# Performance work log

Measured on AMD Instinct MI355X. Metric: run time of the kernel, lower is better.

The kernel has to match this reference:

```python
import jax, jax.numpy as jnp
import numpy as np

# Episode configuration (matches init_kwargs); feature map fixed by module: [64,7,7]
N_WAY, K_SHOT, Q_QUERY, PRJ = 10, 5, 100, 16
DIM, H, W = 64, 7, 7
N_SUP = N_WAY * K_SHOT * PRJ      # 800 support samples
N_QRY = N_WAY * Q_QUERY * PRJ     # 16000 query samples
B = N_SUP + N_QRY                 # 16800
TRIU_I, TRIU_J = np.triu_indices(DIM)  # row-major upper-tri indices, matches torch nonzero order


def setup_inputs() -> dict:
    key = jax.random.key(0)
    k1, k2 = jax.random.split(key)
    feat = jax.random.normal(k1, (B, DIM, H, W), dtype=jnp.float32)
    label = jax.random.randint(k2, (N_QRY,), 0, N_WAY, dtype=jnp.int64)
    # nn.Parameter init: log(1/(2*h*w)) * ones(1,1)
    temp = jnp.log(jnp.ones((1, 1), dtype=jnp.float32) / (2.0 * H * W))
    return {"feat": feat, "temp": temp, "label": label}


def _bdcovpool(x, t):
    # x: [B, dim, h, w] -> Brownian distance covariance matrix [B, dim, dim]
    b, d, h, w = x.shape
    xm = x.reshape(b, d, h * w)
    g = jnp.einsum('bim,bjm->bij', xm, xm)            # x @ x^T, [B,d,d]
    dg = jnp.diagonal(g, axis1=1, axis2=2)            # [B,d]
    # I_M @ (G*I) + (G*I) @ I_M - 2G  ==  diag_j + diag_i - 2G
    dcov = dg[:, None, :] + dg[:, :, None] - 2.0 * g
    dcov = jnp.sqrt(jnp.exp(t) * jnp.clip(dcov, 0.0) + 1e-5)
    # double centering: dcov - rowmean - colmean + totalmean
    rm = jnp.mean(dcov, axis=2, keepdims=True)        # (1/d) dcov @ I_M
    cm = jnp.mean(dcov, axis=1, keepdims=True)        # (1/d) I_M @ dcov
    tm = jnp.mean(dcov, axis=(1, 2), keepdims=True)   # (1/d^2) I_M @ dcov @ I_M
    return dcov - rm - cm + tm


def reference(feat, temp, label):
    v = _bdcovpool(feat, temp)                        # [B, 64, 64]
    tv = v[:, TRIU_I, TRIU_J]                         # Triuvec: [B, 2080]
    support = tv[:N_SUP].reshape(N_WAY, K_SHOT * PRJ, -1).mean(axis=1)  # [n_way, 2080]
    query = tv[N_SUP:]                                # [N_QRY, 2080]
    # negative squared euclidean distance (expanded form of sum((x-y)^2))
    q2 = jnp.sum(query * query, axis=1, keepdims=True)          # [N_QRY,1]
    s2 = jnp.sum(support * support, axis=1)[None, :]             # [1,n_way]
    score = -(q2 + s2 - 2.0 * jnp.einsum('nd,md->nm', query, support))  # [N_QRY, n_way]
    logp = jax.nn.log_softmax(score, axis=-1)
    loss = -jnp.mean(jnp.take_along_axis(logp, label[:, None], axis=1))
    return score, loss
```

## Files before the change

### kernel.cpp

```cpp
#include <hip/hip_runtime.h>
#include <math.h>

#define NWAY   10
#define DIMD   64
#define HWN    49
#define NSUP   800
#define NQRY   16000
#define NTRI   2080
#define FEAT_PER (DIMD*HWN)
#define STP    12

typedef __attribute__((ext_vector_type(8))) short bf16x8;
typedef __attribute__((ext_vector_type(4))) float f32x4;

struct __align__(16) BDCShared {
    union {
        unsigned short hl[2*DIMD*64];
        float dcov[DIMD*64];
        float part[256*12];
    } u;
    float dg[DIMD];
    float rm[DIMD];
    float w4[4];
    float red[16];
};

__device__ __forceinline__ void k2ij(int k, int& io, int& jo) {
    int ii = (int)floorf((129.0f - sqrtf(16641.0f - 8.0f*(float)k)) * 0.5f);
    int off = ii*(129-ii)/2;
    if (off > k) { --ii; off = ii*(129-ii)/2; }
    else {
        int off2 = (ii+1)*(128-ii)/2;
        if (off2 <= k) { ii += 1; off = off2; }
    }
    io = ii;
    jo = ii + (k - off);
}

__device__ __forceinline__ unsigned cvt_pk_bf16(float a, float b) {
    unsigned r;
    asm("v_cvt_pk_bf16_f32 %0, %1, %2" : "=v"(r) : "v"(a), "v"(b));
    return r;
}

#define HL_ADDR(BASE, row, e) \
    ((BASE) + (row)*64 + (((((e) >> 3) ^ ((row) & 7))) << 3))

__device__ __forceinline__ float bdc_compute(const float* __restrict__ feat,
                                             float et, int sample, BDCShared& sm,
                                             f32x4& v0, f32x4& v1, f32x4& v2,
                                             f32x4& v3) {
    const int tid = threadIdx.x;
    unsigned short* Hh = sm.u.hl;
    unsigned short* Lh = sm.u.hl + DIMD*64;

    {
        const int d = tid & 63, hq = tid >> 6;
        const float* rowp = feat + (size_t)sample * FEAT_PER + d*HWN + hq*16;
        float x[16];
        if (hq < 3) {
            #pragma unroll
            for (int i = 0; i < 16; ++i) x[i] = rowp[i];
        } else {
            x[0] = rowp[0];
            #pragma unroll
            for (int i = 1; i < 16; ++i) x[i] = 0.0f;
        }
        unsigned hp[8], lp[8];
        #pragma unroll
        for (int i = 0; i < 8; ++i) {
            unsigned h = cvt_pk_bf16(x[2*i], x[2*i+1]);
            float h0 = __uint_as_float(h << 16);
            float h1 = __uint_as_float(h & 0xffff0000u);
            hp[i] = h;
            lp[i] = cvt_pk_bf16(x[2*i] - h0, x[2*i+1] - h1);
        }
        const int sw0 = (hq*2)     ^ (d & 7);
        const int sw1 = (hq*2 + 1) ^ (d & 7);
        *(uint4*)&Hh[d*64 + sw0*8] = make_uint4(hp[0], hp[1], hp[2], hp[3]);
        *(uint4*)&Hh[d*64 + sw1*8] = make_uint4(hp[4], hp[5], hp[6], hp[7]);
        *(uint4*)&Lh[d*64 + sw0*8] = make_uint4(lp[0], lp[1], lp[2], lp[3]);
        *(uint4*)&Lh[d*64 + sw1*8] = make_uint4(lp[4], lp[5], lp[6], lp[7]);
    }
    __syncthreads();

    const int wv = tid >> 6, lane = tid & 63;
    const int qd = lane >> 4, c15 = lane & 15;
    const int rA = 16*wv + c15;
    bf16x8 AH0 = *(const bf16x8*)HL_ADDR(Hh, rA, qd*8);
    bf16x8 AH1 = *(const bf16x8*)HL_ADDR(Hh, rA, qd*8 + 32);
    bf16x8 AL0 = *(const bf16x8*)HL_ADDR(Lh, rA, qd*8);
    bf16x8 AL1 = *(const bf16x8*)HL_ADDR(Lh, rA, qd*8 + 32);

    f32x4 acc[4];
    #pragma unroll
    for (int J = 0; J < 4; ++J) {
        const int rB = 16*J + c15;
        bf16x8 BH0 = *(const bf16x8*)HL_ADDR(Hh, rB, qd*8);
        bf16x8 BH1 = *(const bf16x8*)HL_ADDR(Hh, rB, qd*8 + 32);
        bf16x8 BL0 = *(const bf16x8*)HL_ADDR(Lh, rB, qd*8);
        bf16x8 BL1 = *(const bf16x8*)HL_ADDR(Lh, rB, qd*8 + 32);
        f32x4 a = {0.f, 0.f, 0.f, 0.f};
        a = __builtin_amdgcn_mfma_f32_16x16x32_bf16(AH0, BH0, a, 0, 0, 0);
        a = __builtin_amdgcn_mfma_f32_16x16x32_bf16(AH1, BH1, a, 0, 0, 0);
        a = __builtin_amdgcn_mfma_f32_16x16x32_bf16(AL0, BH0, a, 0, 0, 0);
        a = __builtin_amdgcn_mfma_f32_16x16x32_bf16(AL1, BH1, a, 0, 0, 0);
        a = __builtin_amdgcn_mfma_f32_16x16x32_bf16(AH0, BL0, a, 0, 0, 0);
        a = __builtin_amdgcn_mfma_f32_16x16x32_bf16(AH1, BL1, a, 0, 0, 0);
        acc[J] = a;
    }

    #pragma unroll
    for (int J = 0; J < 4; ++J) {
        if (J == wv) {
            #pragma unroll
            for (int r = 0; r < 4; ++r)
                if (c15 == 4*qd + r) sm.dg[16*wv + c15] = acc[J][r];
        }
    }
    __syncthreads();

    f32x4 dgi = *(const f32x4*)&sm.dg[16*wv + 4*qd];
    float rs0 = 0.f, rs1 = 0.f, rs2 = 0.f, rs3 = 0.f;
#define DCOV_J(J, VJ)                                                          \
    {   float dgj = sm.dg[16*(J) + c15];                                       \
        _Pragma("unroll")                                                      \
        for (int r = 0; r < 4; ++r) {                                          \
            float t2 = fmaf(-2.0f, acc[J][r], dgi[r] + dgj);                   \
            t2 = fmaxf(t2, 0.0f);                                              \
            VJ[r] = __builtin_amdgcn_sqrtf(fmaf(et, t2, 1e-5f));               \
        }                                                                      \
        rs0 += VJ[0]; rs1 += VJ[1]; rs2 += VJ[2]; rs3 += VJ[3]; }
    DCOV_J(0, v0)
    DCOV_J(1, v1)
    DCOV_J(2, v2)
    DCOV_J(3, v3)
#undef DCOV_J

    #pragma unroll
    for (int off = 1; off < 16; off <<= 1) {
        rs0 += __shfl_xor(rs0, off, 64);
        rs1 += __shfl_xor(rs1, off, 64);
        rs2 += __shfl_xor(rs2, off, 64);
        rs3 += __shfl_xor(rs3, off, 64);
    }
    if (c15 == 0) {
        f32x4 rmv = {rs0*(1.0f/64.0f), rs1*(1.0f/64.0f),
                     rs2*(1.0f/64.0f), rs3*(1.0f/64.0f)};
        *(f32x4*)&sm.rm[16*wv + 4*qd] = rmv;
    }
    float tt = (rs0 + rs1) + (rs2 + rs3);
    tt += __shfl_xor(tt, 16, 64);
    tt += __shfl_xor(tt, 32, 64);
    if (lane == 0) sm.w4[wv] = tt;
    __syncthreads();
    float tm = (sm.w4[0] + sm.w4[1] + sm.w4[2] + sm.w4[3]) * (1.0f/4096.0f);

    const float rmi0 = rs0*(1.0f/64.0f), rmi1 = rs1*(1.0f/64.0f),
                rmi2 = rs2*(1.0f/64.0f), rmi3 = rs3*(1.0f/64.0f);
    float* dcovf = sm.u.dcov;
    const int cch = 4*wv + qd;
#define CENTER_J(J, VJ)                                                        \
    {   int j16 = 16*(J) + c15;                                                \
        float rmj = sm.rm[j16] - tm;                                           \
        VJ[0] = VJ[0] - rmi0 - rmj;                                            \
        VJ[1] = VJ[1] - rmi1 - rmj;                                            \
        VJ[2] = VJ[2] - rmi2 - rmj;                                            \
        VJ[3] = VJ[3] - rmi3 - rmj;                                            \
        *(f32x4*)&dcovf[j16*64 + ((cch ^ (j16 & 7)) << 2)] = VJ; }
    CENTER_J(0, v0)
    CENTER_J(1, v1)
    CENTER_J(2, v2)
    CENTER_J(3, v3)
#undef CENTER_J
    __syncthreads();
    return tm;
}

__global__ void kern_init(unsigned* __restrict__ table,
                          float* __restrict__ s2,
                          float* __restrict__ loss_slot) {
    int i = blockIdx.x * 256 + threadIdx.x;
    if (i < NTRI) {
        int ii, jj; k2ij(i, ii, jj);
        unsigned faddr = (unsigned)(jj*64 + ((((ii >> 2) ^ (jj & 7)) << 2) | (ii & 3)));
        table[i] = (faddr << 16) | ((unsigned)ii << 8) | (unsigned)jj;
    }
    if (i < NWAY) s2[i] = 0.0f;
    if (i == 0) loss_slot[0] = 0.0f;
}

__global__ __launch_bounds__(256, 8) void kern_support(const float* __restrict__ feat,
                                                       const float* __restrict__ temp,
                                                       float* __restrict__ tvout) {
    __shared__ BDCShared sm;
    float et = __expf(temp[0]);
    int s = blockIdx.x;
    f32x4 v0, v1, v2, v3;
    bdc_compute(feat, et, s, sm, v0, v1, v2, v3);

    const int tid = threadIdx.x;
    const int wv = tid >> 6, lane = tid & 63;
    const int qd = lane >> 4, c15 = lane & 15;
    const int iB = 16*wv + 4*qd;
    float* dst = tvout + (size_t)s * NTRI;
#define SUP_J(J, VJ)                                                           \
    {   int j = 16*(J) + c15;                                                  \
        _Pragma("unroll")                                                      \
        for (int r = 0; r < 4; ++r) {                                          \
            int i = iB + r;                                                    \
            if (j >= i) dst[i*(129 - i)/2 + (j - i)] = VJ[r]; } }
    SUP_J(0, v0)
    SUP_J(1, v1)
    SUP_J(2, v2)
    SUP_J(3, v3)
#undef SUP_J
}

__global__ __launch_bounds__(256) void kern_reduce(const float* __restrict__ tv,
                                                   const unsigned* __restrict__ table,
                                                   float* __restrict__ supT,
                                                   float* __restrict__ s2) {
    __shared__ float red[4];
    int m = blockIdx.x / 9, kc = blockIdx.x % 9;
    int k = kc*256 + threadIdx.x;
    float S = 0.0f;
    if (k < NTRI) {
        const float* p = tv + (size_t)(80*m) * NTRI + k;
        float a0 = 0.f, a1 = 0.f, a2 = 0.f, a3 = 0.f;
        for (int s4 = 0; s4 < 80; s4 += 4) {
            a0 += p[(size_t)(s4+0)*NTRI];
            a1 += p[(size_t)(s4+1)*NTRI];
            a2 += p[(size_t)(s4+2)*NTRI];
            a3 += p[(size_t)(s4+3)*NTRI];
        }
        S = ((a0+a1)+(a2+a3)) * (1.0f/80.0f);
        supT[k*STP + m] = S;
    }
    float ps = S * S;
    int lane = threadIdx.x & 63, wv = threadIdx.x >> 6;
    #pragma unroll
    for (int off = 32; off > 0; off >>= 1) ps += __shfl_xor(ps, off, 64);
    if (lane == 0) red[wv] = ps;
    __syncthreads();
    if (threadIdx.x == 0) atomicAdd(&s2[m], red[0]+red[1]+red[2]+red[3]);
}

__global__ __launch_bounds__(256, 8) void kern_query(const float* __restrict__ feat,
                                                     const float* __restrict__ temp,
                                                     const unsigned* __restrict__ table,
                                                     const float* __restrict__ supT,
                                                     const float* __restrict__ s2,
                                                     float* __restrict__ out) {
    __shared__ BDCShared sm;
    float et = __expf(temp[0]);
    int qn = blockIdx.x;
    f32x4 v0, v1, v2, v3;
    bdc_compute(feat, et, NSUP + qn, sm, v0, v1, v2, v3);

    const int tid = threadIdx.x;
    float qq = 0.0f;
    float cr[NWAY];
    #pragma unroll
    for (int m = 0; m < NWAY; ++m) cr[m] = 0.0f;

    const float* dcov = sm.u.dcov;
    for (int k = tid; k < NTRI; k += 256) {
        unsigned t = table[k];
        float v = dcov[t >> 16];
        qq = fmaf(v, v, qq);
        const float4* sp = (const float4*)(supT + (size_t)k * STP);
        float4 sa = sp[0], sb = sp[1], sc = sp[2];
        cr[0] = fmaf(v, sa.x, cr[0]);
        cr[1] = fmaf(v, sa.y, cr[1]);
        cr[2] = fmaf(v, sa.z, cr[2]);
        cr[3] = fmaf(v, sa.w, cr[3]);
        cr[4] = fmaf(v, sb.x, cr[4]);
        cr[5] = fmaf(v, sb.y, cr[5]);
        cr[6] = fmaf(v, sb.z, cr[6]);
        cr[7] = fmaf(v, sb.w, cr[7]);
        cr[8] = fmaf(v, sc.x, cr[8]);
        cr[9] = fmaf(v, sc.y, cr[9]);
    }
    __syncthreads();

    float* part = sm.u.part;
    f32x4 p0 = {cr[0], cr[1], cr[2], cr[3]};
    f32x4 p1 = {cr[4], cr[5], cr[6], cr[7]};
    f32x4 p2 = {cr[8], cr[9], qq, 0.0f};
    *(f32x4*)&part[tid*12 + 0] = p0;
    *(f32x4*)&part[tid*12 + 4] = p1;
    *(f32x4*)&part[tid*12 + 8] = p2;
    __syncthreads();
    if (tid < 176) {
        int m = tid >> 4, g = tid & 15;
        float s = 0.0f;
        #pragma unroll
        for (int t = 0; t < 16; ++t) s += part[(g + 16*t)*12 + m];
        #pragma unroll
        for (int off = 1; off < 16; off <<= 1) s += __shfl_xor(s, off, 64);
        if (g == 0) sm.red[m] = s;
    }
    __syncthreads();
    if (tid < NWAY)
        out[(size_t)qn * NWAY + tid] = -(sm.red[10] + s2[tid] - 2.0f*sm.red[tid]);
}

__global__ __launch_bounds__(256) void kern_loss(const float* __restrict__ score,
                                                 const int* __restrict__ label,
                                                 float* __restrict__ loss_out) {
    __shared__ float red[4];
    int n = blockIdx.x * 256 + threadIdx.x;
    float lsum = 0.0f;
    if (n < NQRY) {
        const float* srow = score + (size_t)n * NWAY;
        float s[NWAY];
        float mx = -1e30f;
        #pragma unroll
        for (int m = 0; m < NWAY; ++m) { s[m] = srow[m]; mx = fmaxf(mx, s[m]); }
        float se = 0.0f;
        #pragma unroll
        for (int m = 0; m < NWAY; ++m) se += __expf(s[m] - mx);
        float lse = mx + __logf(se);
        lsum = lse - s[label[n]];
    }
    int lane = threadIdx.x & 63, wv = threadIdx.x >> 6;
    #pragma unroll
    for (int off = 32; off > 0; off >>= 1) lsum += __shfl_xor(lsum, off, 64);
    if (lane == 0) red[wv] = lsum;
    __syncthreads();
    if (threadIdx.x == 0)
        atomicAdd(loss_out, (red[0] + red[1] + red[2] + red[3]) * (1.0f / (float)NQRY));
}

extern "C" void kernel_launch(void* const* d_in, const int* in_sizes, int n_in,
                              void* d_out, int out_size, void* d_ws, size_t ws_size,
                              hipStream_t stream) {
    (void)in_sizes; (void)n_in; (void)out_size; (void)ws_size;
    const float* feat = (const float*)d_in[0];
    const float* temp = (const float*)d_in[1];
    const int*   label = (const int*)d_in[2];
    float* out = (float*)d_out;

    float*    tv    = (float*)d_ws;
    float*    supT  = tv + (size_t)NSUP * NTRI;
    float*    s2    = supT + NTRI*STP;
    unsigned* table = (unsigned*)(s2 + 16);
    float* loss_slot = out + (size_t)NQRY * NWAY;

    kern_init<<<(NTRI + 255)/256, 256, 0, stream>>>(table, s2, loss_slot);
    kern_support<<<NSUP, 256, 0, stream>>>(feat, temp, tv);
    kern_reduce<<<NWAY*9, 256, 0, stream>>>(tv, table, supT, s2);
    kern_query<<<NQRY, 256, 0, stream>>>(feat, temp, table, supT, s2, out);
    kern_loss<<<(NQRY + 255)/256, 256, 0, stream>>>(out, label, loss_slot);
}
```

Baseline: 351.2 us.

## Process two query samples per block in kern_query to amortize support loads

kern_query now handles two query samples per 256-thread block, staging both feature maps into double shared-memory regions and interleaving their Gram, dcov, centering and score accumulation. Each supT row and table entry loaded from global memory is reused for both queries, halving the support/table traffic and the number of barriers per sample. In exchange shared memory and register use roughly double, and launch bounds drop from 8 to 4 blocks per CU, which lowers occupancy and latency hiding.

Measured after the change: 337.4 us. 3.9% less time.

```diff
diff --git a/kernel.cpp b/kernel.cpp
--- a/kernel.cpp
+++ b/kernel.cpp
@@ -25,6 +25,20 @@
     float red[16];
 };
 
+struct __align__(16) BDC2Shared {
+    union Reg {
+        unsigned short hl[2*DIMD*64];
+        float dcov[DIMD*64];
+        float part[256*12];
+    };
+    Reg r0;
+    Reg r1;
+    float dg0[DIMD], dg1[DIMD];
+    float rm0[DIMD], rm1[DIMD];
+    float w40[4], w41[4];
+    float red0[16], red1[16];
+};
+
 __device__ __forceinline__ void k2ij(int k, int& io, int& jo) {
     int ii = (int)floorf((129.0f - sqrtf(16641.0f - 8.0f*(float)k)) * 0.5f);
     int off = ii*(129-ii)/2;
@@ -46,69 +60,93 @@
 #define HL_ADDR(BASE, row, e) \
     ((BASE) + (row)*64 + (((((e) >> 3) ^ ((row) & 7))) << 3))
 
+
+#define STAGE_Q(HLBASE, SAMPLE)                                                \
+    {   const float* rowp = feat + (size_t)(SAMPLE)*FEAT_PER + d*HWN + hq*16;  \
+        float x[16];                                                           \
+        if (hq < 3) {                                                          \
+            _Pragma("unroll")                                                  \
+            for (int i = 0; i < 16; ++i) x[i] = rowp[i];                       \
+        } else {                                                               \
+            x[0] = rowp[0];                                                    \
+            _Pragma("unroll")                                                  \
+            for (int i = 1; i < 16; ++i) x[i] = 0.0f;                          \
+        }                                                                      \
+        unsigned hp[8], lp[8];                                                 \
+        _Pragma("unroll")                                                      \
+        for (int i = 0; i < 8; ++i) {                                          \
+            unsigned h = cvt_pk_bf16(x[2*i], x[2*i+1]);                        \
+            float h0 = __uint_as_float(h << 16);                               \
+            float h1 = __uint_as_float(h & 0xffff0000u);                       \
+            hp[i] = h;                                                         \
+            lp[i] = cvt_pk_bf16(x[2*i] - h0, x[2*i+1] - h1);                   \
+        }                                                                      \
+        unsigned short* Hq = (HLBASE);                                         \
+        unsigned short* Lq = (HLBASE) + DIMD*64;                               \
+        *(uint4*)&Hq[d*64 + sw0*8] = make_uint4(hp[0], hp[1], hp[2], hp[3]);   \
+        *(uint4*)&Hq[d*64 + sw1*8] = make_uint4(hp[4], hp[5], hp[6], hp[7]);   \
+        *(uint4*)&Lq[d*64 + sw0*8] = make_uint4(lp[0], lp[1], lp[2], lp[3]);   \
+        *(uint4*)&Lq[d*64 + sw1*8] = make_uint4(lp[4], lp[5], lp[6], lp[7]); }
+
+#define GRAM_Q(HLBASE, ACC)                                                    \
+    {   unsigned short* Hq = (HLBASE);                                         \
+        unsigned short* Lq = (HLBASE) + DIMD*64;                               \
+        bf16x8 AH0 = *(const bf16x8*)HL_ADDR(Hq, rA, qd*8);                    \
+        bf16x8 AH1 = *(const bf16x8*)HL_ADDR(Hq, rA, qd*8 + 32);               \
+        bf16x8 AL0 = *(const bf16x8*)HL_ADDR(Lq, rA, qd*8);                    \
+        bf16x8 AL1 = *(const bf16x8*)HL_ADDR(Lq, rA, qd*8 + 32);               \
+        _Pragma("unroll")                                                      \
+        for (int J = 0; J < 4; ++J) {                                          \
+            const int rB = 16*J + c15;                                         \
+            bf16x8 BH0 = *(const bf16x8*)HL_ADDR(Hq, rB, qd*8);                \
+            bf16x8 BH1 = *(const bf16x8*)HL_ADDR(Hq, rB, qd*8 + 32);           \
+            bf16x8 BL0 = *(const bf16x8*)HL_ADDR(Lq, rB, qd*8);                \
+            bf16x8 BL1 = *(const bf16x8*)HL_ADDR(Lq, rB, qd*8 + 32);           \
+            f32x4 a = {0.f, 0.f, 0.f, 0.f};                                    \
+            a = __builtin_amdgcn_mfma_f32_16x16x32_bf16(AH0, BH0, a, 0, 0, 0); \
+            a = __builtin_amdgcn_mfma_f32_16x16x32_bf16(AH1, BH1, a, 0, 0, 0); \
+            a = __builtin_amdgcn_mfma_f32_16x16x32_bf16(AL0, BH0, a, 0, 0, 0); \
+            a = __builtin_amdgcn_mfma_f32_16x16x32_bf16(AL1, BH1, a, 0, 0, 0); \
+            a = __builtin_amdgcn_mfma_f32_16x16x32_bf16(AH0, BL0, a, 0, 0, 0); \
+            a = __builtin_amdgcn_mfma_f32_16x16x32_bf16(AH1, BL1, a, 0, 0, 0); \
+            ACC[J] = a;                                                        \
+        } }
+
+#define DCOV_J(J, VJ, ACC, DGARR, DGI, RS0, RS1, RS2, RS3)                     \
+    {   float dgj = (DGARR)[16*(J) + c15];                                     \
+        _Pragma("unroll")                                                      \
+        for (int r = 0; r < 4; ++r) {                                          \
+            float t2 = fmaf(-2.0f, ACC[J][r], (DGI)[r] + dgj);                 \
+            t2 = fmaxf(t2, 0.0f);                                              \
+            VJ[r] = __builtin_amdgcn_sqrtf(fmaf(et, t2, 1e-5f));               \
+        }                                                                      \
+        RS0 += VJ[0]; RS1 += VJ[1]; RS2 += VJ[2]; RS3 += VJ[3]; }
+
+#define CENTER_J(J, VJ, RMARR, DCOVF, TM, RMI0, RMI1, RMI2, RMI3)              \
+    {   int j16 = 16*(J) + c15;                                                \
+        float rmj = (RMARR)[j16] - (TM);                                       \
+        VJ[0] = VJ[0] - (RMI0) - rmj;                                          \
+        VJ[1] = VJ[1] - (RMI1) - rmj;                                          \
+        VJ[2] = VJ[2] - (RMI2) - rmj;                                          \
+        VJ[3] = VJ[3] - (RMI3) - rmj;                                          \
+        *(f32x4*)&(DCOVF)[j16*64 + ((cch ^ (j16 & 7)) << 2)] = VJ; }
+
 __device__ __forceinline__ float bdc_compute(const float* __restrict__ feat,
                                              float et, int sample, BDCShared& sm,
                                              f32x4& v0, f32x4& v1, f32x4& v2,
                                              f32x4& v3) {
     const int tid = threadIdx.x;
-    unsigned short* Hh = sm.u.hl;
-    unsigned short* Lh = sm.u.hl + DIMD*64;
-
-    {
-        const int d = tid & 63, hq = tid >> 6;
-        const float* rowp = feat + (size_t)sample * FEAT_PER + d*HWN + hq*16;
-        float x[16];
-        if (hq < 3) {
-            #pragma unroll
-            for (int i = 0; i < 16; ++i) x[i] = rowp[i];
-        } else {
-            x[0] = rowp[0];
-            #pragma unroll
-            for (int i = 1; i < 16; ++i) x[i] = 0.0f;
-        }
-        unsigned hp[8], lp[8];
-        #pragma unroll
-        for (int i = 0; i < 8; ++i) {
-            unsigned h = cvt_pk_bf16(x[2*i], x[2*i+1]);
-            float h0 = __uint_as_float(h << 16);
-            float h1 = __uint_as_float(h & 0xffff0000u);
-            hp[i] = h;
-            lp[i] = cvt_pk_bf16(x[2*i] - h0, x[2*i+1] - h1);
-        }
-        const int sw0 = (hq*2)     ^ (d & 7);
-        const int sw1 = (hq*2 + 1) ^ (d & 7);
-        *(uint4*)&Hh[d*64 + sw0*8] = make_uint4(hp[0], hp[1], hp[2], hp[3]);
-        *(uint4*)&Hh[d*64 + sw1*8] = make_uint4(hp[4], hp[5], hp[6], hp[7]);
-        *(uint4*)&Lh[d*64 + sw0*8] = make_uint4(lp[0], lp[1], lp[2], lp[3]);
-        *(uint4*)&Lh[d*64 + sw1*8] = make_uint4(lp[4], lp[5], lp[6], lp[7]);
-    }
+    const int d = tid & 63, hq = tid >> 6;
+    const int sw0 = (hq*2) ^ (d & 7);
+    const int sw1 = (hq*2 + 1) ^ (d & 7);
+    STAGE_Q(sm.u.hl, sample)
     __syncthreads();
 
     const int wv = tid >> 6, lane = tid & 63;
     const int qd = lane >> 4, c15 = lane & 15;
     const int rA = 16*wv + c15;
-    bf16x8 AH0 = *(const bf16x8*)HL_ADDR(Hh, rA, qd*8);
-    bf16x8 AH1 = *(const bf16x8*)HL_ADDR(Hh, rA, qd*8 + 32);
-    bf16x8 AL0 = *(const bf16x8*)HL_ADDR(Lh, rA, qd*8);
-    bf16x8 AL1 = *(const bf16x8*)HL_ADDR(Lh, rA, qd*8 + 32);
-
     f32x4 acc[4];
-    #pragma unroll
-    for (int J = 0; J < 4; ++J) {
-        const int rB = 16*J + c15;
-        bf16x8 BH0 = *(const bf16x8*)HL_ADDR(Hh, rB, qd*8);
-        bf16x8 BH1 = *(const bf16x8*)HL_ADDR(Hh, rB, qd*8 + 32);
-        bf16x8 BL0 = *(const bf16x8*)HL_ADDR(Lh, rB, qd*8);
-        bf16x8 BL1 = *(const bf16x8*)HL_ADDR(Lh, rB, qd*8 + 32);
-        f32x4 a = {0.f, 0.f, 0.f, 0.f};
-        a = __builtin_amdgcn_mfma_f32_16x16x32_bf16(AH0, BH0, a, 0, 0, 0);
-        a = __builtin_amdgcn_mfma_f32_16x16x32_bf16(AH1, BH1, a, 0, 0, 0);
-        a = __builtin_amdgcn_mfma_f32_16x16x32_bf16(AL0, BH0, a, 0, 0, 0);
-        a = __builtin_amdgcn_mfma_f32_16x16x32_bf16(AL1, BH1, a, 0, 0, 0);
-        a = __builtin_amdgcn_mfma_f32_16x16x32_bf16(AH0, BL0, a, 0, 0, 0);
-        a = __builtin_amdgcn_mfma_f32_16x16x32_bf16(AH1, BL1, a, 0, 0, 0);
-        acc[J] = a;
-    }
+    GRAM_Q(sm.u.hl, acc)
 
     #pragma unroll
     for (int J = 0; J < 4; ++J) {
@@ -122,20 +160,10 @@
 
     f32x4 dgi = *(const f32x4*)&sm.dg[16*wv + 4*qd];
     float rs0 = 0.f, rs1 = 0.f, rs2 = 0.f, rs3 = 0.f;
-#define DCOV_J(J, VJ)                                                          \
-    {   float dgj = sm.dg[16*(J) + c15];                                       \
-        _Pragma("unroll")                                                      \
-        for (int r = 0; r < 4; ++r) {                                          \
-            float t2 = fmaf(-2.0f, acc[J][r], dgi[r] + dgj);                   \
-            t2 = fmaxf(t2, 0.0f);                                              \
-            VJ[r] = __builtin_amdgcn_sqrtf(fmaf(et, t2, 1e-5f));               \
-        }                                                                      \
-        rs0 += VJ[0]; rs1 += VJ[1]; rs2 += VJ[2]; rs3 += VJ[3]; }
-    DCOV_J(0, v0)
-    DCOV_J(1, v1)
-    DCOV_J(2, v2)
-    DCOV_J(3, v3)
-#undef DCOV_J
+    DCOV_J(0, v0, acc, sm.dg, dgi, rs0, rs1, rs2, rs3)
+    DCOV_J(1, v1, acc, sm.dg, dgi, rs0, rs1, rs2, rs3)
+    DCOV_J(2, v2, acc, sm.dg, dgi, rs0, rs1, rs2, rs3)
+    DCOV_J(3, v3, acc, sm.dg, dgi, rs0, rs1, rs2, rs3)
 
     #pragma unroll
     for (int off = 1; off < 16; off <<= 1) {
@@ -160,19 +188,10 @@
                 rmi2 = rs2*(1.0f/64.0f), rmi3 = rs3*(1.0f/64.0f);
     float* dcovf = sm.u.dcov;
     const int cch = 4*wv + qd;
-#define CENTER_J(J, VJ)                                                        \
-    {   int j16 = 16*(J) + c15;                                                \
-        float rmj = sm.rm[j16] - tm;                                           \
-        VJ[0] = VJ[0] - rmi0 - rmj;                                            \
-        VJ[1] = VJ[1] - rmi1 - rmj;                                            \
-        VJ[2] = VJ[2] - rmi2 - rmj;                                            \
-        VJ[3] = VJ[3] - rmi3 - rmj;                                            \
-        *(f32x4*)&dcovf[j16*64 + ((cch ^ (j16 & 7)) << 2)] = VJ; }
-    CENTER_J(0, v0)
-    CENTER_J(1, v1)
-    CENTER_J(2, v2)
-    CENTER_J(3, v3)
-#undef CENTER_J
+    CENTER_J(0, v0, sm.rm, dcovf, tm, rmi0, rmi1, rmi2, rmi3)
+    CENTER_J(1, v1, sm.rm, dcovf, tm, rmi0, rmi1, rmi2, rmi3)
+    CENTER_J(2, v2, sm.rm, dcovf, tm, rmi0, rmi1, rmi2, rmi3)
+    CENTER_J(3, v3, sm.rm, dcovf, tm, rmi0, rmi1, rmi2, rmi3)
     __syncthreads();
     return tm;
 }
@@ -246,64 +265,175 @@
     if (threadIdx.x == 0) atomicAdd(&s2[m], red[0]+red[1]+red[2]+red[3]);
 }
 
-__global__ __launch_bounds__(256, 8) void kern_query(const float* __restrict__ feat,
+__global__ __launch_bounds__(256, 4) void kern_query(const float* __restrict__ feat,
                                                      const float* __restrict__ temp,
                                                      const unsigned* __restrict__ table,
                                                      const float* __restrict__ supT,
                                                      const float* __restrict__ s2,
                                                      float* __restrict__ out) {
-    __shared__ BDCShared sm;
+    __shared__ BDC2Shared sm;
     float et = __expf(temp[0]);
-    int qn = blockIdx.x;
-    f32x4 v0, v1, v2, v3;
-    bdc_compute(feat, et, NSUP + qn, sm, v0, v1, v2, v3);
-
+    const int qn0 = blockIdx.x * 2;
+    const int qn1 = qn0 + 1;
     const int tid = threadIdx.x;
-    float qq = 0.0f;
-    float cr[NWAY];
-    #pragma unroll
-    for (int m = 0; m < NWAY; ++m) cr[m] = 0.0f;
-
-    const float* dcov = sm.u.dcov;
+
+    {
+        const int d = tid & 63, hq = tid >> 6;
+        const int sw0 = (hq*2) ^ (d & 7);
+        const int sw1 = (hq*2 + 1) ^ (d & 7);
+        STAGE_Q(sm.r0.hl, NSUP + qn0)
+        STAGE_Q(sm.r1.hl, NSUP + qn1)
+    }
+    __syncthreads();
+
+    const int wv = tid >> 6, lane = tid & 63;
+    const int qd = lane >> 4, c15 = lane & 15;
+    const int rA = 16*wv + c15;
+    f32x4 acc0[4], acc1[4];
+    GRAM_Q(sm.r0.hl, acc0)
+    GRAM_Q(sm.r1.hl, acc1)
+
+    #pragma unroll
+    for (int J = 0; J < 4; ++J) {
+        if (J == wv) {
+            #pragma unroll
+            for (int r = 0; r < 4; ++r)
+                if (c15 == 4*qd + r) {
+                    sm.dg0[16*wv + c15] = acc0[J][r];
+                    sm.dg1[16*wv + c15] = acc1[J][r];
+                }
+        }
+    }
+    __syncthreads();
+
+    f32x4 dgi0 = *(const f32x4*)&sm.dg0[16*wv + 4*qd];
+    f32x4 dgi1 = *(const f32x4*)&sm.dg1[16*wv + 4*qd];
+    f32x4 v00, v01, v02, v03, v10, v11, v12, v13;
+    float rs00 = 0.f, rs01 = 0.f, rs02 = 0.f, rs03 = 0.f;
+    float rs10 = 0.f, rs11 = 0.f, rs12 = 0.f, rs13 = 0.f;
+    DCOV_J(0, v00, acc0, sm.dg0, dgi0, rs00, rs01, rs02, rs03)
+    DCOV_J(1, v01, acc0, sm.dg0, dgi0, rs00, rs01, rs02, rs03)
+    DCOV_J(2, v02, acc0, sm.dg0, dgi0, rs00, rs01, rs02, rs03)
+    DCOV_J(3, v03, acc0, sm.dg0, dgi0, rs00, rs01, rs02, rs03)
+    DCOV_J(0, v10, acc1, sm.dg1, dgi1, rs10, rs11, rs12, rs13)
+    DCOV_J(1, v11, acc1, sm.dg1, dgi1, rs10, rs11, rs12, rs13)
+    DCOV_J(2, v12, acc1, sm.dg1, dgi1, rs10, rs11, rs12, rs13)
+    DCOV_J(3, v13, acc1, sm.dg1, dgi1, rs10, rs11, rs12, rs13)
+
+    #pragma unroll
+    for (int off = 1; off < 16; off <<= 1) {
+        rs00 += __shfl_xor(rs00, off, 64);
+        rs01 += __shfl_xor(rs01, off, 64);
+        rs02 += __shfl_xor(rs02, off, 64);
+        rs03 += __shfl_xor(rs03, off, 64);
+        rs10 += __shfl_xor(rs10, off, 64);
+        rs11 += __shfl_xor(rs11, off, 64);
+        rs12 += __shfl_xor(rs12, off, 64);
+        rs13 += __shfl_xor(rs13, off, 64);
+    }
+    if (c15 == 0) {
+        f32x4 rmv0 = {rs00*(1.0f/64.0f), rs01*(1.0f/64.0f),
+                      rs02*(1.0f/64.0f), rs03*(1.0f/64.0f)};
+        f32x4 rmv1 = {rs10*(1.0f/64.0f), rs11*(1.0f/64.0f),
+                      rs12*(1.0f/64.0f), rs13*(1.0f/64.0f)};
+        *(f32x4*)&sm.rm0[16*wv + 4*qd] = rmv0;
+        *(f32x4*)&sm.rm1[16*wv + 4*qd] = rmv1;
+    }
+    float tt0 = (rs00 + rs01) + (rs02 + rs03);
+    float tt1 = (rs10 + rs11) + (rs12 + rs13);
+    tt0 += __shfl_xor(tt0, 16, 64);
+    tt0 += __shfl_xor(tt0, 32, 64);
+    tt1 += __shfl_xor(tt1, 16, 64);
+    tt1 += __shfl_xor(tt1, 32, 64);
+    if (lane == 0) { sm.w40[wv] = tt0; sm.w41[wv] = tt1; }
+    __syncthreads();
+    float tm0 = (sm.w40[0] + sm.w40[1] + sm.w40[2] + sm.w40[3]) * (1.0f/4096.0f);
+    float tm1 = (sm.w41[0] + sm.w41[1] + sm.w41[2] + sm.w41[3]) * (1.0f/4096.0f);
+
+    {
+        const float rmi00 = rs00*(1.0f/64.0f), rmi01 = rs01*(1.0f/64.0f),
+                    rmi02 = rs02*(1.0f/64.0f), rmi03 = rs03*(1.0f/64.0f);
+        const float rmi10 = rs10*(1.0f/64.0f), rmi11 = rs11*(1.0f/64.0f),
+                    rmi12 = rs12*(1.0f/64.0f), rmi13 = rs13*(1.0f/64.0f);
+        float* dc0 = sm.r0.dcov;
+        float* dc1 = sm.r1.dcov;
+        const int cch = 4*wv + qd;
+        CENTER_J(0, v00, sm.rm0, dc0, tm0, rmi00, rmi01, rmi02, rmi03)
+        CENTER_J(1, v01, sm.rm0, dc0, tm0, rmi00, rmi01, rmi02, rmi03)
+        CENTER_J(2, v02, sm.rm0, dc0, tm0, rmi00, rmi01, rmi02, rmi03)
+        CENTER_J(3, v03, sm.rm0, dc0, tm0, rmi00, rmi01, rmi02, rmi03)
+        CENTER_J(0, v10, sm.rm1, dc1, tm1, rmi10, rmi11, rmi12, rmi13)
+        CENTER_J(1, v11, sm.rm1, dc1, tm1, rmi10, rmi11, rmi12, rmi13)
+        CENTER_J(2, v12, sm.rm1, dc1, tm1, rmi10, rmi11, rmi12, rmi13)
+        CENTER_J(3, v13, sm.rm1, dc1, tm1, rmi10, rmi11, rmi12, rmi13)
+    }
+    __syncthreads();
+
+    float qq0 = 0.0f, qq1 = 0.0f;
+    float cr0[NWAY], cr1[NWAY];
+    #pragma unroll
+    for (int m = 0; m < NWAY; ++m) { cr0[m] = 0.0f; cr1[m] = 0.0f; }
+
+    const float* dcov0 = sm.r0.dcov;
+    const float* dcov1 = sm.r1.dcov;
     for (int k = tid; k < NTRI; k += 256) {
         unsigned t = table[k];
-        float v = dcov[t >> 16];
-        qq = fmaf(v, v, qq);
+        float va = dcov0[t >> 16];
+        float vb = dcov1[t >> 16];
+        qq0 = fmaf(va, va, qq0);
+        qq1 = fmaf(vb, vb, qq1);
         const float4* sp = (const float4*)(supT + (size_t)k * STP);
         float4 sa = sp[0], sb = sp[1], sc = sp[2];
-        cr[0] = fmaf(v, sa.x, cr[0]);
-        cr[1] = fmaf(v, sa.y, cr[1]);
-        cr[2] = fmaf(v, sa.z, cr[2]);
-        cr[3] = fmaf(v, sa.w, cr[3]);
-        cr[4] = fmaf(v, sb.x, cr[4]);
-        cr[5] = fmaf(v, sb.y, cr[5]);
-        cr[6] = fmaf(v, sb.z, cr[6]);
-        cr[7] = fmaf(v, sb.w, cr[7]);
-        cr[8] = fmaf(v, sc.x, cr[8]);
-        cr[9] = fmaf(v, sc.y, cr[9]);
-    }
-    __syncthreads();
-
-    float* part = sm.u.part;
-    f32x4 p0 = {cr[0], cr[1], cr[2], cr[3]};
-    f32x4 p1 = {cr[4], cr[5], cr[6], cr[7]};
-    f32x4 p2 = {cr[8], cr[9], qq, 0.0f};
-    *(f32x4*)&part[tid*12 + 0] = p0;
-    *(f32x4*)&part[tid*12 + 4] = p1;
-    *(f32x4*)&part[tid*12 + 8] = p2;
+        cr0[0] = fmaf(va, sa.x, cr0[0]);  cr1[0] = fmaf(vb, sa.x, cr1[0]);
+        cr0[1] = fmaf(va, sa.y, cr0[1]);  cr1[1] = fmaf(vb, sa.y, cr1[1]);
+        cr0[2] = fmaf(va, sa.z, cr0[2]);  cr1[2] = fmaf(vb, sa.z, cr1[2]);
+        cr0[3] = fmaf(va, sa.w, cr0[3]);  cr1[3] = fmaf(vb, sa.w, cr1[3]);
+        cr0[4] = fmaf(va, sb.x, cr0[4]);  cr1[4] = fmaf(vb, sb.x, cr1[4]);
+        cr0[5] = fmaf(va, sb.y, cr0[5]);  cr1[5] = fmaf(vb, sb.y, cr1[5]);
+        cr0[6] = fmaf(va, sb.z, cr0[6]);  cr1[6] = fmaf(vb, sb.z, cr1[6]);
+        cr0[7] = fmaf(va, sb.w, cr0[7]);  cr1[7] = fmaf(vb, sb.w, cr1[7]);
+        cr0[8] = fmaf(va, sc.x, cr0[8]);  cr1[8] = fmaf(vb, sc.x, cr1[8]);
+        cr0[9] = fmaf(va, sc.y, cr0[9]);  cr1[9] = fmaf(vb, sc.y, cr1[9]);
+    }
+    __syncthreads();
+
+    float* part0 = (float*)&sm.r0;
+    float* part1 = (float*)&sm.r1;
+    {
+        f32x4 p0 = {cr0[0], cr0[1], cr0[2], cr0[3]};
+        f32x4 p1 = {cr0[4], cr0[5], cr0[6], cr0[7]};
+        f32x4 p2 = {cr0[8], cr0[9], qq0, 0.0f};
+        *(f32x4*)&part0[tid*12 + 0] = p0;
+        *(f32x4*)&part0[tid*12 + 4] = p1;
+        *(f32x4*)&part0[tid*12 + 8] = p2;
+        f32x4 p3 = {cr1[0], cr1[1], cr1[2], cr1[3]};
+        f32x4 p4 = {cr1[4], cr1[5], cr1[6], cr1[7]};
+        f32x4 p5 = {cr1[8], cr1[9], qq1, 0.0f};
+        *(f32x4*)&part1[tid*12 + 0] = p3;
+        *(f32x4*)&part1[tid*12 + 4] = p4;
+        *(f32x4*)&part1[tid*12 + 8] = p5;
+    }
     __syncthreads();
     if (tid < 176) {
         int m = tid >> 4, g = tid & 15;
-        float s = 0.0f;
+        float sA = 0.0f, sB = 0.0f;
         #pragma unroll
-        for (int t = 0; t < 16; ++t) s += part[(g + 16*t)*12 + m];
+        for (int t = 0; t < 16; ++t) {
+            sA += part0[(g + 16*t)*12 + m];
+            sB += part1[(g + 16*t)*12 + m];
+        }
         #pragma unroll
-        for (int off = 1; off < 16; off <<= 1) s += __shfl_xor(s, off, 64);
-        if (g == 0) sm.red[m] = s;
-    }
-    __syncthreads();
-    if (tid < NWAY)
-        out[(size_t)qn * NWAY + tid] = -(sm.red[10] + s2[tid] - 2.0f*sm.red[tid]);
+        for (int off = 1; off < 16; off <<= 1) {
+            sA += __shfl_xor(sA, off, 64);
+            sB += __shfl_xor(sB, off, 64);
+        }
+        if (g == 0) { sm.red0[m] = sA; sm.red1[m] = sB; }
+    }
+    __syncthreads();
+    if (tid < NWAY) {
+        out[(size_t)qn0 * NWAY + tid] = -(sm.red0[10] + s2[tid] - 2.0f*sm.red0[tid]);
+        out[(size_t)qn1 * NWAY + tid] = -(sm.red1[10] + s2[tid] - 2.0f*sm.red1[tid]);
+    }
 }
 
 __global__ __launch_bounds__(256) void kern_loss(const float* __restrict__ score,
@@ -351,6 +481,6 @@
     kern_init<<<(NTRI + 255)/256, 256, 0, stream>>>(table, s2, loss_slot);
     kern_support<<<NSUP, 256, 0, stream>>>(feat, temp, tv);
     kern_reduce<<<NWAY*9, 256, 0, stream>>>(tv, table, supT, s2);
-    kern_query<<<NQRY, 256, 0, stream>>>(feat, temp, table, supT, s2, out);
+    kern_query<<<NQRY/2, 256, 0, stream>>>(feat, temp, table, supT, s2, out);
     kern_loss<<<(NQRY + 255)/256, 256, 0, stream>>>(out, label, loss_slot);
 }
```

## Compute each query's covariance in one wavefront with full symmetric support dot and fused loss

Applied to the files above, without the earlier changes.

The query kernel is rewritten so each wavefront handles one query sample entirely in registers. Features are loaded directly into MFMA operands, and the Gram matrix, distance, centering and squared norm are computed without block-wide LDS staging or barriers. The support means are stored as full symmetric 64x64 matrices, so the query dot product runs over all entries with halved off-diagonal weights instead of a triangle gather through a lookup table. The loss kernel is folded into the query kernel and the init kernel into the support kernel, which removes launches, at the cost of higher register pressure (launch bounds drop to 3) and an atomic per query.

Result: slower. 632.5 us (+80.1%).

```diff
diff --git a/kernel.cpp b/kernel.cpp
--- a/kernel.cpp
+++ b/kernel.cpp
@@ -8,7 +8,6 @@
 #define NQRY   16000
 #define NTRI   2080
 #define FEAT_PER (DIMD*HWN)
-#define STP    12
 
 typedef __attribute__((ext_vector_type(8))) short bf16x8;
 typedef __attribute__((ext_vector_type(4))) float f32x4;
@@ -17,12 +16,10 @@
     union {
         unsigned short hl[2*DIMD*64];
         float dcov[DIMD*64];
-        float part[256*12];
     } u;
     float dg[DIMD];
     float rm[DIMD];
     float w4[4];
-    float red[16];
 };
 
 __device__ __forceinline__ void k2ij(int k, int& io, int& jo) {
@@ -43,6 +40,21 @@
     return r;
 }
 
+__device__ __forceinline__ void pack_hl(const float* x, bf16x8& H, bf16x8& L) {
+    unsigned hh[4], ll[4];
+    #pragma unroll
+    for (int p = 0; p < 4; ++p) {
+        unsigned h = cvt_pk_bf16(x[2*p], x[2*p+1]);
+        float f0 = __uint_as_float(h << 16);
+        float f1 = __uint_as_float(h & 0xffff0000u);
+        hh[p] = h;
+        ll[p] = cvt_pk_bf16(x[2*p] - f0, x[2*p+1] - f1);
+    }
+    union { uint4 u; bf16x8 b; } cu;
+    cu.u = make_uint4(hh[0], hh[1], hh[2], hh[3]); H = cu.b;
+    cu.u = make_uint4(ll[0], ll[1], ll[2], ll[3]); L = cu.b;
+}
+
 #define HL_ADDR(BASE, row, e) \
     ((BASE) + (row)*64 + (((((e) >> 3) ^ ((row) & 7))) << 3))
 
@@ -53,7 +65,6 @@
     const int tid = threadIdx.x;
     unsigned short* Hh = sm.u.hl;
     unsigned short* Lh = sm.u.hl + DIMD*64;
-
     {
         const int d = tid & 63, hq = tid >> 6;
         const float* rowp = feat + (size_t)sample * FEAT_PER + d*HWN + hq*16;
@@ -66,21 +77,15 @@
             #pragma unroll
             for (int i = 1; i < 16; ++i) x[i] = 0.0f;
         }
-        unsigned hp[8], lp[8];
-        #pragma unroll
-        for (int i = 0; i < 8; ++i) {
-            unsigned h = cvt_pk_bf16(x[2*i], x[2*i+1]);
-            float h0 = __uint_as_float(h << 16);
-            float h1 = __uint_as_float(h & 0xffff0000u);
-            hp[i] = h;
-            lp[i] = cvt_pk_bf16(x[2*i] - h0, x[2*i+1] - h1);
-        }
-        const int sw0 = (hq*2)     ^ (d & 7);
+        bf16x8 hA, lA, hB, lB;
+        pack_hl(x, hA, lA);
+        pack_hl(x + 8, hB, lB);
+        const int sw0 = (hq*2) ^ (d & 7);
         const int sw1 = (hq*2 + 1) ^ (d & 7);
-        *(uint4*)&Hh[d*64 + sw0*8] = make_uint4(hp[0], hp[1], hp[2], hp[3]);
-        *(uint4*)&Hh[d*64 + sw1*8] = make_uint4(hp[4], hp[5], hp[6], hp[7]);
-        *(uint4*)&Lh[d*64 + sw0*8] = make_uint4(lp[0], lp[1], lp[2], lp[3]);
-        *(uint4*)&Lh[d*64 + sw1*8] = make_uint4(lp[4], lp[5], lp[6], lp[7]);
+        *(bf16x8*)&Hh[d*64 + sw0*8] = hA;
+        *(bf16x8*)&Hh[d*64 + sw1*8] = hB;
+        *(bf16x8*)&Lh[d*64 + sw0*8] = lA;
+        *(bf16x8*)&Lh[d*64 + sw1*8] = lB;
     }
     __syncthreads();
 
@@ -158,48 +163,43 @@
 
     const float rmi0 = rs0*(1.0f/64.0f), rmi1 = rs1*(1.0f/64.0f),
                 rmi2 = rs2*(1.0f/64.0f), rmi3 = rs3*(1.0f/64.0f);
-    float* dcovf = sm.u.dcov;
-    const int cch = 4*wv + qd;
 #define CENTER_J(J, VJ)                                                        \
-    {   int j16 = 16*(J) + c15;                                                \
-        float rmj = sm.rm[j16] - tm;                                           \
+    {   float rmj = sm.rm[16*(J) + c15] - tm;                                  \
         VJ[0] = VJ[0] - rmi0 - rmj;                                            \
         VJ[1] = VJ[1] - rmi1 - rmj;                                            \
         VJ[2] = VJ[2] - rmi2 - rmj;                                            \
-        VJ[3] = VJ[3] - rmi3 - rmj;                                            \
-        *(f32x4*)&dcovf[j16*64 + ((cch ^ (j16 & 7)) << 2)] = VJ; }
+        VJ[3] = VJ[3] - rmi3 - rmj; }
     CENTER_J(0, v0)
     CENTER_J(1, v1)
     CENTER_J(2, v2)
     CENTER_J(3, v3)
 #undef CENTER_J
-    __syncthreads();
     return tm;
-}
-
-__global__ void kern_init(unsigned* __restrict__ table,
-                          float* __restrict__ s2,
-                          float* __restrict__ loss_slot) {
-    int i = blockIdx.x * 256 + threadIdx.x;
-    if (i < NTRI) {
-        int ii, jj; k2ij(i, ii, jj);
-        unsigned faddr = (unsigned)(jj*64 + ((((ii >> 2) ^ (jj & 7)) << 2) | (ii & 3)));
-        table[i] = (faddr << 16) | ((unsigned)ii << 8) | (unsigned)jj;
-    }
-    if (i < NWAY) s2[i] = 0.0f;
-    if (i == 0) loss_slot[0] = 0.0f;
 }
 
 __global__ __launch_bounds__(256, 8) void kern_support(const float* __restrict__ feat,
                                                        const float* __restrict__ temp,
-                                                       float* __restrict__ tvout) {
+                                                       float* __restrict__ tvout,
+                                                       unsigned* __restrict__ table,
+                                                       float* __restrict__ s2,
+                                                       float* __restrict__ loss_slot) {
+    const int tid = threadIdx.x;
+    if (blockIdx.x < 9) {
+        int i = blockIdx.x * 256 + tid;
+        if (i < NTRI) {
+            int ii, jj; k2ij(i, ii, jj);
+            table[i] = ((unsigned)ii << 8) | (unsigned)jj;
+        }
+        if (i < NWAY) s2[i] = 0.0f;
+        if (i == 0) loss_slot[0] = 0.0f;
+    }
+
     __shared__ BDCShared sm;
     float et = __expf(temp[0]);
     int s = blockIdx.x;
     f32x4 v0, v1, v2, v3;
     bdc_compute(feat, et, s, sm, v0, v1, v2, v3);
 
-    const int tid = threadIdx.x;
     const int wv = tid >> 6, lane = tid & 63;
     const int qd = lane >> 4, c15 = lane & 15;
     const int iB = 16*wv + 4*qd;
@@ -219,12 +219,12 @@
 
 __global__ __launch_bounds__(256) void kern_reduce(const float* __restrict__ tv,
                                                    const unsigned* __restrict__ table,
-                                                   float* __restrict__ supT,
+                                                   float* __restrict__ Sfull,
                                                    float* __restrict__ s2) {
     __shared__ float red[4];
     int m = blockIdx.x / 9, kc = blockIdx.x % 9;
     int k = kc*256 + threadIdx.x;
-    float S = 0.0f;
+    float ps = 0.0f;
     if (k < NTRI) {
         const float* p = tv + (size_t)(80*m) * NTRI + k;
         float a0 = 0.f, a1 = 0.f, a2 = 0.f, a3 = 0.f;
@@ -234,10 +234,14 @@
             a2 += p[(size_t)(s4+2)*NTRI];
             a3 += p[(size_t)(s4+3)*NTRI];
         }
-        S = ((a0+a1)+(a2+a3)) * (1.0f/80.0f);
-        supT[k*STP + m] = S;
-    }
-    float ps = S * S;
+        float S = ((a0+a1)+(a2+a3)) * (1.0f/80.0f);
+        unsigned t = table[k];
+        int ii = (int)((t >> 8) & 255u), jj = (int)(t & 255u);
+        float* Sm = Sfull + (size_t)m * 4096;
+        Sm[ii*64 + jj] = S;
+        Sm[jj*64 + ii] = S;
+        ps = S * S;
+    }
     int lane = threadIdx.x & 63, wv = threadIdx.x >> 6;
     #pragma unroll
     for (int off = 32; off > 0; off >>= 1) ps += __shfl_xor(ps, off, 64);
@@ -246,91 +250,207 @@
     if (threadIdx.x == 0) atomicAdd(&s2[m], red[0]+red[1]+red[2]+red[3]);
 }
 
-__global__ __launch_bounds__(256, 8) void kern_query(const float* __restrict__ feat,
+__global__ __launch_bounds__(256, 3) void kern_query(const float* __restrict__ feat,
                                                      const float* __restrict__ temp,
-                                                     const unsigned* __restrict__ table,
-                                                     const float* __restrict__ supT,
+                                                     const float* __restrict__ Sfull,
                                                      const float* __restrict__ s2,
-                                                     float* __restrict__ out) {
-    __shared__ BDCShared sm;
-    float et = __expf(temp[0]);
-    int qn = blockIdx.x;
-    f32x4 v0, v1, v2, v3;
-    bdc_compute(feat, et, NSUP + qn, sm, v0, v1, v2, v3);
-
+                                                     const int* __restrict__ label,
+                                                     float* __restrict__ out,
+                                                     float* __restrict__ loss_out) {
+    __shared__ float dgrm[4][136];
     const int tid = threadIdx.x;
-    float qq = 0.0f;
+    const int w = tid >> 6, lane = tid & 63;
+    const int qd = lane >> 4, c15 = lane & 15;
+    const float et = __expf(temp[0]);
+    const int qn = blockIdx.x * 4 + w;
+    const float* fp = feat + (size_t)(NSUP + qn) * FEAT_PER;
+
+    bf16x8 fH0[4], fH1[4], fL0[4], fL1[4];
+    #pragma unroll
+    for (int J = 0; J < 4; ++J) {
+        const float* rp = fp + (16*J + c15)*HWN;
+        float xa[8], xb[8];
+        #pragma unroll
+        for (int t = 0; t < 8; ++t) {
+            xa[t] = rp[qd*8 + t];
+            int k = 32 + qd*8 + t;
+            xb[t] = (k < HWN) ? rp[k] : 0.0f;
+        }
+        pack_hl(xa, fH0[J], fL0[J]);
+        pack_hl(xb, fH1[J], fL1[J]);
+    }
+
+    f32x4 acc[4][4];
+    #pragma unroll
+    for (int I = 0; I < 4; ++I) {
+        #pragma unroll
+        for (int J = 0; J < 4; ++J) {
+            f32x4 a = {0.f, 0.f, 0.f, 0.f};
+            a = __builtin_amdgcn_mfma_f32_16x16x32_bf16(fH0[I], fH0[J], a, 0, 0, 0);
+            a = __builtin_amdgcn_mfma_f32_16x16x32_bf16(fH1[I], fH1[J], a, 0, 0, 0);
+            a = __builtin_amdgcn_mfma_f32_16x16x32_bf16(fL0[I], fH0[J], a, 0, 0, 0);
+            a = __builtin_amdgcn_mfma_f32_16x16x32_bf16(fL1[I], fH1[J], a, 0, 0, 0);
+            a = __builtin_amdgcn_mfma_f32_16x16x32_bf16(fH0[I], fL0[J], a, 0, 0, 0);
+            a = __builtin_amdgcn_mfma_f32_16x16x32_bf16(fH1[I], fL1[J], a, 0, 0, 0);
+            acc[I][J] = a;
+        }
+    }
+
+    #pragma unroll
+    for (int I = 0; I < 4; ++I) {
+        #pragma unroll
+        for (int r = 0; r < 4; ++r)
+            if (c15 == 4*qd + r) dgrm[w][16*I + c15] = acc[I][I][r];
+    }
+    asm volatile("s_waitcnt lgkmcnt(0)" ::: "memory");
+    f32x4 dgi[4];
+    float dgj[4];
+    #pragma unroll
+    for (int I = 0; I < 4; ++I) dgi[I] = *(const f32x4*)&dgrm[w][16*I + 4*qd];
+    #pragma unroll
+    for (int J = 0; J < 4; ++J) dgj[J] = dgrm[w][16*J + c15];
+
+    f32x4 vt[4][4];
+    float rsum[4][4];
+    #pragma unroll
+    for (int I = 0; I < 4; ++I) {
+        #pragma unroll
+        for (int r = 0; r < 4; ++r) rsum[I][r] = 0.0f;
+    }
+    #pragma unroll
+    for (int I = 0; I < 4; ++I) {
+        #pragma unroll
+        for (int J = 0; J < 4; ++J) {
+            #pragma unroll
+            for (int r = 0; r < 4; ++r) {
+                float t2 = fmaf(-2.0f, acc[I][J][r], dgi[I][r] + dgj[J]);
+                t2 = fmaxf(t2, 0.0f);
+                float sv = __builtin_amdgcn_sqrtf(fmaf(et, t2, 1e-5f));
+                vt[I][J][r] = sv;
+                rsum[I][r] += sv;
+            }
+        }
+    }
+    #pragma unroll
+    for (int off = 1; off < 16; off <<= 1) {
+        #pragma unroll
+        for (int I = 0; I < 4; ++I) {
+            #pragma unroll
+            for (int r = 0; r < 4; ++r)
+                rsum[I][r] += __shfl_xor(rsum[I][r], off, 64);
+        }
+    }
+    float tot = 0.0f;
+    #pragma unroll
+    for (int I = 0; I < 4; ++I) {
+        #pragma unroll
+        for (int r = 0; r < 4; ++r) tot += rsum[I][r];
+    }
+    tot += __shfl_xor(tot, 16, 64);
+    tot += __shfl_xor(tot, 32, 64);
+    const float tm = tot * (1.0f/4096.0f);
+    const float inv64 = 1.0f/64.0f;
+
+    if (c15 == 0) {
+        #pragma unroll
+        for (int I = 0; I < 4; ++I) {
+            f32x4 rmv = {rsum[I][0]*inv64, rsum[I][1]*inv64,
+                         rsum[I][2]*inv64, rsum[I][3]*inv64};
+            *(f32x4*)&dgrm[w][64 + 16*I + 4*qd] = rmv;
+        }
+    }
+    asm volatile("s_waitcnt lgkmcnt(0)" ::: "memory");
+    float rmj[4];
+    #pragma unroll
+    for (int J = 0; J < 4; ++J) rmj[J] = dgrm[w][64 + 16*J + c15];
+
+    #pragma unroll
+    for (int I = 0; I < 4; ++I) {
+        #pragma unroll
+        for (int J = 0; J < 4; ++J) {
+            #pragma unroll
+            for (int r = 0; r < 4; ++r)
+                vt[I][J][r] = 0.5f*(vt[I][J][r] - rsum[I][r]*inv64 - rmj[J] + tm);
+        }
+    }
+    float dadj = 0.0f;
+    #pragma unroll
+    for (int I = 0; I < 4; ++I) {
+        if (qd == (c15 >> 2)) {
+            #pragma unroll
+            for (int r = 0; r < 4; ++r)
+                if ((c15 & 3) == r) {
+                    vt[I][I][r] *= 2.0f;
+                    dadj += vt[I][I][r]*vt[I][I][r];
+                }
+        }
+    }
+    float qq2 = 0.0f;
+    #pragma unroll
+    for (int I = 0; I < 4; ++I) {
+        #pragma unroll
+        for (int J = 0; J < 4; ++J) {
+            #pragma unroll
+            for (int r = 0; r < 4; ++r)
+                qq2 = fmaf(vt[I][J][r], vt[I][J][r], qq2);
+        }
+    }
+    float qq = 2.0f*qq2 - dadj;
+
     float cr[NWAY];
     #pragma unroll
     for (int m = 0; m < NWAY; ++m) cr[m] = 0.0f;
-
-    const float* dcov = sm.u.dcov;
-    for (int k = tid; k < NTRI; k += 256) {
-        unsigned t = table[k];
-        float v = dcov[t >> 16];
-        qq = fmaf(v, v, qq);
-        const float4* sp = (const float4*)(supT + (size_t)k * STP);
-        float4 sa = sp[0], sb = sp[1], sc = sp[2];
-        cr[0] = fmaf(v, sa.x, cr[0]);
-        cr[1] = fmaf(v, sa.y, cr[1]);
-        cr[2] = fmaf(v, sa.z, cr[2]);
-        cr[3] = fmaf(v, sa.w, cr[3]);
-        cr[4] = fmaf(v, sb.x, cr[4]);
-        cr[5] = fmaf(v, sb.y, cr[5]);
-        cr[6] = fmaf(v, sb.z, cr[6]);
-        cr[7] = fmaf(v, sb.w, cr[7]);
-        cr[8] = fmaf(v, sc.x, cr[8]);
-        cr[9] = fmaf(v, sc.y, cr[9]);
-    }
-    __syncthreads();
-
-    float* part = sm.u.part;
-    f32x4 p0 = {cr[0], cr[1], cr[2], cr[3]};
-    f32x4 p1 = {cr[4], cr[5], cr[6], cr[7]};
-    f32x4 p2 = {cr[8], cr[9], qq, 0.0f};
-    *(f32x4*)&part[tid*12 + 0] = p0;
-    *(f32x4*)&part[tid*12 + 4] = p1;
-    *(f32x4*)&part[tid*12 + 8] = p2;
-    __syncthreads();
-    if (tid < 176) {
-        int m = tid >> 4, g = tid & 15;
-        float s = 0.0f;
-        #pragma unroll
-        for (int t = 0; t < 16; ++t) s += part[(g + 16*t)*12 + m];
-        #pragma unroll
-        for (int off = 1; off < 16; off <<= 1) s += __shfl_xor(s, off, 64);
-        if (g == 0) sm.red[m] = s;
-    }
-    __syncthreads();
-    if (tid < NWAY)
-        out[(size_t)qn * NWAY + tid] = -(sm.red[10] + s2[tid] - 2.0f*sm.red[tid]);
-}
-
-__global__ __launch_bounds__(256) void kern_loss(const float* __restrict__ score,
-                                                 const int* __restrict__ label,
-                                                 float* __restrict__ loss_out) {
-    __shared__ float red[4];
-    int n = blockIdx.x * 256 + threadIdx.x;
-    float lsum = 0.0f;
-    if (n < NQRY) {
-        const float* srow = score + (size_t)n * NWAY;
-        float s[NWAY];
-        float mx = -1e30f;
-        #pragma unroll
-        for (int m = 0; m < NWAY; ++m) { s[m] = srow[m]; mx = fmaxf(mx, s[m]); }
+    #pragma unroll
+    for (int J = 0; J < 4; ++J) {
+        #pragma unroll
+        for (int I = 0; I < 4; ++I) {
+            const float* sp = Sfull + (16*J + c15)*64 + 16*I + 4*qd;
+            #pragma unroll
+            for (int m = 0; m < NWAY; ++m) {
+                f32x4 sf = *(const f32x4*)(sp + m*4096);
+                cr[m] = fmaf(vt[I][J][0], sf[0], cr[m]);
+                cr[m] = fmaf(vt[I][J][1], sf[1], cr[m]);
+                cr[m] = fmaf(vt[I][J][2], sf[2], cr[m]);
+                cr[m] = fmaf(vt[I][J][3], sf[3], cr[m]);
+            }
+        }
+    }
+
+    #pragma unroll
+    for (int m = 0; m < NWAY; ++m) {
+        float v = cr[m];
+        #pragma unroll
+        for (int off = 1; off < 64; off <<= 1) v += __shfl_xor(v, off, 64);
+        cr[m] = v;
+    }
+    #pragma unroll
+    for (int off = 1; off < 64; off <<= 1) qq += __shfl_xor(qq, off, 64);
+
+    float s2r[NWAY];
+    #pragma unroll
+    for (int m = 0; m < NWAY; ++m) s2r[m] = s2[m];
+
+    #pragma unroll
+    for (int m = 0; m < NWAY; ++m)
+        if (lane == m) out[(size_t)qn * NWAY + m] = -(qq + s2r[m] - 2.0f*cr[m]);
+
+    if (lane == 0) {
+        int lb = label[qn];
+        float mx = -1e30f, tsc = 0.0f;
+        #pragma unroll
+        for (int m = 0; m < NWAY; ++m) {
+            float sc = -(qq + s2r[m] - 2.0f*cr[m]);
+            mx = fmaxf(mx, sc);
+            if (m == lb) tsc = sc;
+        }
         float se = 0.0f;
         #pragma unroll
-        for (int m = 0; m < NWAY; ++m) se += __expf(s[m] - mx);
-        float lse = mx + __logf(se);
-        lsum = lse - s[label[n]];
-    }
-    int lane = threadIdx.x & 63, wv = threadIdx.x >> 6;
-    #pragma unroll
-    for (int off = 32; off > 0; off >>= 1) lsum += __shfl_xor(lsum, off, 64);
-    if (lane == 0) red[wv] = lsum;
-    __syncthreads();
-    if (threadIdx.x == 0)
-        atomicAdd(loss_out, (red[0] + red[1] + red[2] + red[3]) * (1.0f / (float)NQRY));
+        for (int m = 0; m < NWAY; ++m) {
+            float sc = -(qq + s2r[m] - 2.0f*cr[m]);
+            se += __expf(sc - mx);
+        }
+        atomicAdd(loss_out, (mx + __logf(se) - tsc) * (1.0f / (float)NQRY));
+    }
 }
 
 extern "C" void kernel_launch(void* const* d_in, const int* in_sizes, int n_in,
@@ -343,14 +463,12 @@
     float* out = (float*)d_out;
 
     float*    tv    = (float*)d_ws;
-    float*    supT  = tv + (size_t)NSUP * NTRI;
-    float*    s2    = supT + NTRI*STP;
+    float*    Sfull = tv + (size_t)NSUP * NTRI;
+    float*    s2    = Sfull + (size_t)NWAY * 4096;
     unsigned* table = (unsigned*)(s2 + 16);
     float* loss_slot = out + (size_t)NQRY * NWAY;
 
-    kern_init<<<(NTRI + 255)/256, 256, 0, stream>>>(table, s2, loss_slot);
-    kern_support<<<NSUP, 256, 0, stream>>>(feat, temp, tv);
-    kern_reduce<<<NWAY*9, 256, 0, stream>>>(tv, table, supT, s2);
-    kern_query<<<NQRY, 256, 0, stream>>>(feat, temp, table, supT, s2, out);
-    kern_loss<<<(NQRY + 255)/256, 256, 0, stream>>>(out, label, loss_slot);
-}
+    kern_support<<<NSUP, 256, 0, stream>>>(feat, temp, tv, table, s2, loss_slot);
+    kern_reduce<<<NWAY*9, 256, 0, stream>>>(tv, table, Sfull, s2);
+    kern_query<<<NQRY/4, 256, 0, stream>>>(feat, temp, Sfull, s2, label, out, loss_slot);
+}
```
